# Kernel optimization log

Hardware: AMD Instinct MI355X
Metric: run time of the kernel (lower is better)

## Reference

```python
import jax, jax.numpy as jnp
import numpy as np

B, T, C, H = 4, 2048, 1024, 16
D = C // H  # head dim = 64

def setup_inputs() -> dict:
    key = jax.random.key(0)
    k1, k2, k3 = jax.random.split(key, 3)
    s = 1.0 / np.sqrt(C)
    return {
        "x": jax.random.normal(k1, (B, T, C), dtype=jnp.float32),
        "W_attn": jax.random.normal(k2, (C, 3 * C), dtype=jnp.float32) * s,
        "b_attn": jnp.zeros((3 * C,), dtype=jnp.float32),
        "W_proj": jax.random.normal(k3, (C, C), dtype=jnp.float32) * s,
        "b_proj": jnp.zeros((C,), dtype=jnp.float32),
    }

def reference(x, W_attn, b_attn, W_proj, b_proj):
    qkv = x @ W_attn + b_attn                      # [B,T,3C]
    q, k, v = jnp.split(qkv, 3, axis=-1)
    # [B,T,C] -> [B,H,T,D]
    q = q.reshape(B, T, H, D).transpose(0, 2, 1, 3)
    k = k.reshape(B, T, H, D).transpose(0, 2, 1, 3)
    v = v.reshape(B, T, H, D).transpose(0, 2, 1, 3)
    scale = 1.0 / np.sqrt(D)
    att = jnp.einsum('bhqd,bhkd->bhqk', q, k) * scale   # [B,H,T,T]
    causal = jnp.tril(jnp.ones((T, T), dtype=bool))
    att = jnp.where(causal[None, None], att, jnp.float32(-jnp.inf))
    att = jax.nn.softmax(att, axis=-1)
    y = jnp.einsum('bhqk,bhkd->bhqd', att, v)            # [B,H,T,D]
    y = y.transpose(0, 2, 1, 3).reshape(B, T, C)
    return y @ W_proj + b_proj
```

## Files before the change

kernel.cpp:

```cpp
#include <hip/hip_runtime.h>
#include <cstdint>
#include <cstddef>

typedef __bf16 bf16;
typedef __bf16 bf16x8 __attribute__((ext_vector_type(8)));
typedef __bf16 bf16x4 __attribute__((ext_vector_type(4)));
typedef short  s16x4  __attribute__((ext_vector_type(4)));
typedef float  f32x4  __attribute__((ext_vector_type(4)));

#define MFMA16(a, b, c) __builtin_amdgcn_mfma_f32_16x16x32_bf16((a), (b), (c), 0, 0, 0)

#if __has_builtin(__builtin_amdgcn_mfma_f32_16x16x16bf16_1k)
#define HAVE_K16 1
#else
#define HAVE_K16 0
#endif

#if __has_builtin(__builtin_amdgcn_exp2f)
#define EXP2(x) __builtin_amdgcn_exp2f(x)
#else
#define EXP2(x) exp2f(x)
#endif

constexpr int Bsz = 4;
constexpr int T   = 2048;
constexpr int Cd  = 1024;
constexpr int Hn  = 16;
constexpr int Mrows = Bsz * T;
constexpr int QKV_LD = 3 * Cd;

constexpr float QSCALE = 0.125f * 1.4426950408889634f;

__global__ __launch_bounds__(256) void cvt_f32_bf16(const float* __restrict__ in,
                                                    bf16* __restrict__ out, int n) {
    int i = (blockIdx.x * 256 + threadIdx.x) * 8;
    if (i >= n) return;
    float4 a = *(const float4*)(in + i);
    float4 b = *(const float4*)(in + i + 4);
    bf16x8 o;
    o[0] = (bf16)a.x; o[1] = (bf16)a.y; o[2] = (bf16)a.z; o[3] = (bf16)a.w;
    o[4] = (bf16)b.x; o[5] = (bf16)b.y; o[6] = (bf16)b.z; o[7] = (bf16)b.w;
    *(bf16x8*)(out + i) = o;
}

template <int KDIM, int NDIM>
__global__ __launch_bounds__(256) void transpose_cvt(const float* __restrict__ W,
                                                     bf16* __restrict__ Wt) {
    __shared__ float tile[32][33];
    int k0 = blockIdx.y * 32;
    int n0 = blockIdx.x * 32;
    int tx = threadIdx.x;
    int ty = threadIdx.y;
    #pragma unroll
    for (int r = 0; r < 32; r += 8)
        tile[r + ty][tx] = W[(size_t)(k0 + r + ty) * NDIM + n0 + tx];
    __syncthreads();
    #pragma unroll
    for (int r = 0; r < 32; r += 8)
        Wt[(size_t)(n0 + r + ty) * KDIM + k0 + tx] = (bf16)tile[tx][r + ty];
}

template <int N, bool OUT_BF16>
__global__ __launch_bounds__(256) void gemm_bf16(const bf16* __restrict__ A,
                                                 const bf16* __restrict__ Bt,
                                                 const float* __restrict__ bias,
                                                 void* __restrict__ outp,
                                                 float oscale, int oscale_n) {
    constexpr int K = 1024;
    __shared__ __align__(16) bf16 As[128 * 64];
    __shared__ __align__(16) bf16 Bs[128 * 64];

    const int tid  = threadIdx.x;
    const int w    = tid >> 6;
    const int lane = tid & 63;
    const int wm   = w & 1, wn = w >> 1;
    const int quad = lane >> 4, c16 = lane & 15;

    const int lin = (int)(blockIdx.y * gridDim.x + blockIdx.x);
    const int x8  = lin & 7;
    const int q   = lin >> 3;
    const int m0  = (x8 + 8 * (q & 7)) * 128;
    const int n0  = (q >> 3) * 128;

    const int srow = lane >> 3;
    const int scol = ((lane & 7) ^ srow) * 8;
    const int sw   = c16 & 7;

    f32x4 acc[4][4] = {};

    for (int kt = 0; kt < K / 64; ++kt) {
        const int kk = kt * 64;
        #pragma unroll
        for (int i = 0; i < 4; ++i) {
            const int arow = 32 * w + 8 * i;
            __builtin_amdgcn_global_load_lds(
                (const __attribute__((address_space(1))) void*)(A + (size_t)(m0 + arow + srow) * K + kk + scol),
                (__attribute__((address_space(3))) void*)(&As[arow * 64]),
                16, 0, 0);
            __builtin_amdgcn_global_load_lds(
                (const __attribute__((address_space(1))) void*)(Bt + (size_t)(n0 + arow + srow) * K + kk + scol),
                (__attribute__((address_space(3))) void*)(&Bs[arow * 64]),
                16, 0, 0);
        }
        __syncthreads();

        #pragma unroll
        for (int ks = 0; ks < 2; ++ks) {
            const int go = ((ks * 4 + quad) ^ sw) * 8;
            bf16x8 af[4], bfv[4];
            #pragma unroll
            for (int mb = 0; mb < 4; ++mb)
                af[mb] = *(const bf16x8*)&As[(wm * 64 + mb * 16 + c16) * 64 + go];
            #pragma unroll
            for (int nb = 0; nb < 4; ++nb)
                bfv[nb] = *(const bf16x8*)&Bs[(wn * 64 + nb * 16 + c16) * 64 + go];
            #pragma unroll
            for (int mb = 0; mb < 4; ++mb)
                #pragma unroll
                for (int nb = 0; nb < 4; ++nb)
                    acc[mb][nb] = MFMA16(af[mb], bfv[nb], acc[mb][nb]);
        }
        __syncthreads();
    }

    #pragma unroll
    for (int nb = 0; nb < 4; ++nb) {
        const int n = n0 + wn * 64 + nb * 16 + c16;
        const float bv = bias[n];
        const float sc = (n < oscale_n) ? oscale : 1.0f;
        #pragma unroll
        for (int mb = 0; mb < 4; ++mb) {
            const int mbase = m0 + wm * 64 + mb * 16 + quad * 4;
            #pragma unroll
            for (int r = 0; r < 4; ++r) {
                float v = (acc[mb][nb][r] + bv) * sc;
                if (OUT_BF16)
                    ((bf16*)outp)[(size_t)(mbase + r) * N + n] = (bf16)v;
                else
                    ((float*)outp)[(size_t)(mbase + r) * N + n] = v;
            }
        }
    }
}

__global__ __launch_bounds__(256, 2) void attn_fwd(const bf16* __restrict__ qkv,
                                                   bf16* __restrict__ yp0,
                                                   bf16* __restrict__ yp1,
                                                   float* __restrict__ lp) {
    __shared__ __align__(16) bf16 Ks2[2][4096];
    __shared__ __align__(16) bf16 Vs[2][64 * 64];
#if !HAVE_K16
    __shared__ __align__(16) bf16 Ps[4][32 * 72];
#endif

    const int x    = blockIdx.x;
    const int xq   = x >> 1;
    const int sgl  = x & 1;
    const int h    = blockIdx.y;
    const int bb   = blockIdx.z;
    const int tid  = threadIdx.x;
    const int w    = tid >> 6;
    const int lane = tid & 63;
    const int quad = lane >> 4, c16 = lane & 15;

    const size_t base = (size_t)(bb * T) * QKV_LD;

    const int g = tid >> 5;
    const int p = tid & 31;

    auto vs_store = [&](bf16* vbuf, const bf16x8& va, const bf16x8& vb) {
        #pragma unroll
        for (int j = 0; j < 8; ++j) {
            union { bf16 hh[2]; uint32_t u; } pk;
            pk.hh[0] = va[j]; pk.hh[1] = vb[j];
            const int row = 8 * g + j;
            *(uint32_t*)&vbuf[row * 64 + (((p >> 1) ^ (row & 15)) << 2) + ((p & 1) << 1)] = pk.u;
        }
    };

    bf16* __restrict__ ydst = sgl ? yp1 : yp0;
    float* __restrict__ ldst = lp + (size_t)sgl * Mrows * Hn;

    for (int ph = 0; ph < 2; ++ph) {
        const int qt = ph ? xq : (15 - xq);
        const int q0 = qt * 128;
        const int rowbase = q0 + w * 32;
        const int start = sgl ? (qt + 1) : 0;
        const int nkt = qt + 1;

        __syncthreads();

        {
            const int kb = start * 64;
            #pragma unroll
            for (int ii = 0; ii < 2; ++ii) {
                const int i = 2 * w + ii;
                const bf16* gp = qkv + base + (size_t)(kb + 8 * i + (lane & 7)) * QKV_LD + Cd + h * 64 + (lane >> 3) * 8;
                __builtin_amdgcn_global_load_lds(
                    (const __attribute__((address_space(1))) void*)gp,
                    (__attribute__((address_space(3))) void*)(&Ks2[0][i * 512]), 16, 0, 0);
            }
            const bf16* vp = qkv + base + (size_t)(kb + 2 * p) * QKV_LD + 2 * Cd + h * 64 + g * 8;
            bf16x8 va = *(const bf16x8*)vp;
            bf16x8 vb = *(const bf16x8*)(vp + QKV_LD);
            vs_store(Vs[0], va, vb);
        }

        bf16x8 qf[2][2];
        #pragma unroll
        for (int mb = 0; mb < 2; ++mb) {
            const bf16* qp = qkv + base + (size_t)(rowbase + 16 * mb + c16) * QKV_LD + h * 64 + quad * 8;
            qf[mb][0] = *(const bf16x8*)qp;
            qf[mb][1] = *(const bf16x8*)(qp + 32);
        }

        f32x4 yacc[2][4] = {};
        float lsum[2] = {};

        for (int j = 0; j < nkt; ++j) {
            const int cur = j & 1, nxt = cur ^ 1;
            const int k0 = (start + j) * 64;
            __syncthreads();

            bf16x8 va, vb;
            const bool more = (j + 1 < nkt);
            if (more) {
                const int kn = k0 + 64;
                #pragma unroll
                for (int ii = 0; ii < 2; ++ii) {
                    const int i = 2 * w + ii;
                    const bf16* gp = qkv + base + (size_t)(kn + 8 * i + (lane & 7)) * QKV_LD + Cd + h * 64 + (lane >> 3) * 8;
                    __builtin_amdgcn_global_load_lds(
                        (const __attribute__((address_space(1))) void*)gp,
                        (__attribute__((address_space(3))) void*)(&Ks2[nxt][i * 512]), 16, 0, 0);
                }
                const bf16* vp = qkv + base + (size_t)(kn + 2 * p) * QKV_LD + 2 * Cd + h * 64 + g * 8;
                va = *(const bf16x8*)vp;
                vb = *(const bf16x8*)(vp + QKV_LD);
            }

            if (k0 <= rowbase + 31) {
                f32x4 s[2][4] = {};
                __builtin_amdgcn_s_setprio(1);
                #pragma unroll
                for (int ks = 0; ks < 2; ++ks)
                    #pragma unroll
                    for (int blk = 0; blk < 4; ++blk) {
                        const bf16x8 kf = *(const bf16x8*)
                            &Ks2[cur][(2 * blk + (c16 >> 3)) * 512 + (4 * ks + quad) * 64 + (c16 & 7) * 8];
                        #pragma unroll
                        for (int mb = 0; mb < 2; ++mb)
                            s[mb][blk] = MFMA16(kf, qf[mb][ks], s[mb][blk]);
                    }
                __builtin_amdgcn_s_setprio(0);

#if HAVE_K16
                union B4 { bf16x4 v; s16x4 s; } pb[2][4];
#endif
                #pragma unroll
                for (int mb = 0; mb < 2; ++mb) {
                    const int rb = rowbase + 16 * mb;
                    const int qglob = rb + c16;
                    const bool needMask = (k0 + 63 > rb);
                    #pragma unroll
                    for (int blk = 0; blk < 4; ++blk) {
                        #pragma unroll
                        for (int r = 0; r < 4; ++r) {
                            const int key = k0 + blk * 16 + quad * 4 + r;
                            float e = s[mb][blk][r];
                            if (needMask) e = (key > qglob) ? -INFINITY : e;
                            float pv = EXP2(e);
                            lsum[mb] += pv;
#if HAVE_K16
                            pb[mb][blk].v[r] = (bf16)pv;
#else
                            Ps[w][(mb * 16 + c16) * 72 + blk * 16 + quad * 4 + r] = (bf16)pv;
#endif
                        }
                    }
                }

#if HAVE_K16
                __builtin_amdgcn_s_setprio(1);
                #pragma unroll
                for (int blk = 0; blk < 4; ++blk)
                    #pragma unroll
                    for (int d16 = 0; d16 < 4; ++d16) {
                        union B4u { bf16x4 v; s16x4 s; } vf;
                        vf.v = *(const bf16x4*)
                            &Vs[cur][(d16 * 16 + c16) * 64 + ((((blk << 2) | quad) ^ c16) << 2)];
                        #pragma unroll
                        for (int mb = 0; mb < 2; ++mb)
                            yacc[mb][d16] = __builtin_amdgcn_mfma_f32_16x16x16bf16_1k(
                                vf.s, pb[mb][blk].s, yacc[mb][d16], 0, 0, 0);
                    }
                __builtin_amdgcn_s_setprio(0);
#else
                asm volatile("s_waitcnt lgkmcnt(0)" ::: "memory");
                #pragma unroll
                for (int ks = 0; ks < 2; ++ks) {
                    bf16x8 pf0 = *(const bf16x8*)&Ps[w][(0 * 16 + c16) * 72 + ks * 32 + quad * 8];
                    bf16x8 pf1 = *(const bf16x8*)&Ps[w][(1 * 16 + c16) * 72 + ks * 32 + quad * 8];
                    #pragma unroll
                    for (int d16 = 0; d16 < 4; ++d16) {
                        const int row = d16 * 16 + c16;
                        const int g0 = ks * 8 + quad * 2;
                        bf16x4 lo = *(const bf16x4*)&Vs[cur][row * 64 + ((g0 ^ c16) << 2)];
                        bf16x4 hi = *(const bf16x4*)&Vs[cur][row * 64 + (((g0 + 1) ^ c16) << 2)];
                        bf16x8 vfr;
                        vfr[0] = lo[0]; vfr[1] = lo[1]; vfr[2] = lo[2]; vfr[3] = lo[3];
                        vfr[4] = hi[0]; vfr[5] = hi[1]; vfr[6] = hi[2]; vfr[7] = hi[3];
                        yacc[0][d16] = MFMA16(pf0, vfr, yacc[0][d16]);
                        yacc[1][d16] = MFMA16(pf1, vfr, yacc[1][d16]);
                    }
                }
#endif
            }

            if (more)
                vs_store(Vs[nxt], va, vb);
        }

        #pragma unroll
        for (int mb = 0; mb < 2; ++mb) {
            lsum[mb] += __shfl_xor(lsum[mb], 16);
            lsum[mb] += __shfl_xor(lsum[mb], 32);
        }

#if HAVE_K16
        #pragma unroll
        for (int mb = 0; mb < 2; ++mb) {
            const int row = rowbase + 16 * mb + c16;
            bf16* yw = ydst + (size_t)(bb * T + row) * Cd + h * 64;
            #pragma unroll
            for (int d16 = 0; d16 < 4; ++d16) {
                bf16x4 o;
                #pragma unroll
                for (int r = 0; r < 4; ++r)
                    o[r] = (bf16)(yacc[mb][d16][r]);
                *(bf16x4*)(yw + d16 * 16 + quad * 4) = o;
            }
            if (quad == 0)
                ldst[(size_t)(bb * T + row) * Hn + h] = lsum[mb];
        }
#else
        #pragma unroll
        for (int mb = 0; mb < 2; ++mb)
            #pragma unroll
            for (int r = 0; r < 4; ++r) {
                const float lsv = __shfl(lsum[mb], quad * 4 + r);
                const int row = rowbase + 16 * mb + quad * 4 + r;
                bf16* yw = ydst + (size_t)(bb * T + row) * Cd + h * 64;
                #pragma unroll
                for (int d16 = 0; d16 < 4; ++d16)
                    yw[d16 * 16 + c16] = (bf16)(yacc[mb][d16][r]);
                if (c16 == 0)
                    ldst[(size_t)(bb * T + row) * Hn + h] = lsv;
            }
#endif
    }
}

__global__ __launch_bounds__(256) void attn_combine(const bf16* __restrict__ yp0,
                                                    const bf16* __restrict__ yp1,
                                                    const float* __restrict__ lp,
                                                    bf16* __restrict__ y) {
    int i = (blockIdx.x * 256 + threadIdx.x) * 8;
    int row = i >> 10;
    int hh  = (i & 1023) >> 6;
    float l = lp[(size_t)row * Hn + hh] + lp[(size_t)Mrows * Hn + (size_t)row * Hn + hh];
    float inv = 1.f / l;
    bf16x8 a = *(const bf16x8*)(yp0 + i);
    bf16x8 b = *(const bf16x8*)(yp1 + i);
    bf16x8 o;
    #pragma unroll
    for (int j = 0; j < 8; ++j)
        o[j] = (bf16)(((float)a[j] + (float)b[j]) * inv);
    *(bf16x8*)(y + i) = o;
}

extern "C" void kernel_launch(void* const* d_in, const int* in_sizes, int n_in,
                              void* d_out, int out_size, void* d_ws, size_t ws_size,
                              hipStream_t stream) {
    const float* x      = (const float*)d_in[0];
    const float* W_attn = (const float*)d_in[1];
    const float* b_attn = (const float*)d_in[2];
    const float* W_proj = (const float*)d_in[3];
    const float* b_proj = (const float*)d_in[4];
    float* out = (float*)d_out;

    bf16* xb   = (bf16*)d_ws;
    bf16* Wat  = xb  + (size_t)Mrows * Cd;
    bf16* Wpt  = Wat + (size_t)QKV_LD * Cd;
    bf16* qkv  = Wpt + (size_t)Cd * Cd;
    bf16* yb   = qkv + (size_t)Mrows * QKV_LD;
    bf16* yp1  = yb  + (size_t)Mrows * Cd;
    float* lp  = (float*)(yp1 + (size_t)Mrows * Cd);

    cvt_f32_bf16<<<(Mrows * Cd) / (256 * 8), 256, 0, stream>>>(x, xb, Mrows * Cd);
    transpose_cvt<Cd, QKV_LD><<<dim3(QKV_LD / 32, Cd / 32), dim3(32, 8), 0, stream>>>(W_attn, Wat);
    transpose_cvt<Cd, Cd><<<dim3(Cd / 32, Cd / 32), dim3(32, 8), 0, stream>>>(W_proj, Wpt);

    gemm_bf16<QKV_LD, true><<<dim3(QKV_LD / 128, Mrows / 128), 256, 0, stream>>>(
        xb, Wat, b_attn, qkv, QSCALE, Cd);

    attn_fwd<<<dim3(16, Hn, Bsz), 256, 0, stream>>>(qkv, yb, yp1, lp);
    attn_combine<<<(Mrows * Cd) / (256 * 8), 256, 0, stream>>>(yb, yp1, lp, yb);

    gemm_bf16<Cd, false><<<dim3(Cd / 128, Mrows / 128), 256, 0, stream>>>(
        yb, Wpt, b_proj, out, 1.0f, 0);
}
```

Baseline: 288.4 us.

## Split attention key range three ways per query tile and drop setprio hints

The attention kernel now splits each query tile's causal key range across three blocks instead of two, giving 24 x-blocks per head and batch. Each split writes its own partial output and row sum, and the combine kernel adds all three. The third partial buffer and the row-sum array reuse workspace regions (the bf16 input and the weight-transpose area) that are no longer needed at that point. This is meant to raise block count and balance work across CUs. In exchange it adds combine traffic and extra Q loads per block, and it also removes the s_setprio hints around the MFMA loops.

Measured after the change: 275.6 us. 4.4% less time.

```diff
diff --git a/kernel.cpp b/kernel.cpp
--- a/kernel.cpp
+++ b/kernel.cpp
@@ -146,6 +146,7 @@
 __global__ __launch_bounds__(256, 2) void attn_fwd(const bf16* __restrict__ qkv,
                                                    bf16* __restrict__ yp0,
                                                    bf16* __restrict__ yp1,
+                                                   bf16* __restrict__ yp2,
                                                    float* __restrict__ lp) {
     __shared__ __align__(16) bf16 Ks2[2][4096];
     __shared__ __align__(16) bf16 Vs[2][64 * 64];
@@ -154,8 +155,8 @@
 #endif
 
     const int x    = blockIdx.x;
-    const int xq   = x >> 1;
-    const int sgl  = x & 1;
+    const int xq   = x / 3;
+    const int sgl  = x - 3 * xq;
     const int h    = blockIdx.y;
     const int bb   = blockIdx.z;
     const int tid  = threadIdx.x;
@@ -178,15 +179,20 @@
         }
     };
 
-    bf16* __restrict__ ydst = sgl ? yp1 : yp0;
+    bf16* __restrict__ ydst = (sgl == 0) ? yp0 : ((sgl == 1) ? yp1 : yp2);
     float* __restrict__ ldst = lp + (size_t)sgl * Mrows * Hn;
 
     for (int ph = 0; ph < 2; ++ph) {
         const int qt = ph ? xq : (15 - xq);
         const int q0 = qt * 128;
         const int rowbase = q0 + w * 32;
-        const int start = sgl ? (qt + 1) : 0;
-        const int nkt = qt + 1;
+
+        const int n = 2 * qt + 2;
+        int f0, f1;
+        if (ph == 0) { f0 = (n + 2) / 3; f1 = (n + 1) / 3; }
+        else         { f0 = n / 3;       f1 = (n + 1) / 3; }
+        const int start = (sgl == 0) ? 0 : ((sgl == 1) ? f0 : f0 + f1);
+        const int nkt   = (sgl == 0) ? f0 : ((sgl == 1) ? f1 : n - f0 - f1);
 
         __syncthreads();
 
@@ -241,7 +247,6 @@
 
             if (k0 <= rowbase + 31) {
                 f32x4 s[2][4] = {};
-                __builtin_amdgcn_s_setprio(1);
                 #pragma unroll
                 for (int ks = 0; ks < 2; ++ks)
                     #pragma unroll
@@ -252,7 +257,6 @@
                         for (int mb = 0; mb < 2; ++mb)
                             s[mb][blk] = MFMA16(kf, qf[mb][ks], s[mb][blk]);
                     }
-                __builtin_amdgcn_s_setprio(0);
 
 #if HAVE_K16
                 union B4 { bf16x4 v; s16x4 s; } pb[2][4];
@@ -281,7 +285,6 @@
                 }
 
 #if HAVE_K16
-                __builtin_amdgcn_s_setprio(1);
                 #pragma unroll
                 for (int blk = 0; blk < 4; ++blk)
                     #pragma unroll
@@ -294,7 +297,6 @@
                             yacc[mb][d16] = __builtin_amdgcn_mfma_f32_16x16x16bf16_1k(
                                 vf.s, pb[mb][blk].s, yacc[mb][d16], 0, 0, 0);
                     }
-                __builtin_amdgcn_s_setprio(0);
 #else
                 asm volatile("s_waitcnt lgkmcnt(0)" ::: "memory");
                 #pragma unroll
@@ -363,19 +365,23 @@
 
 __global__ __launch_bounds__(256) void attn_combine(const bf16* __restrict__ yp0,
                                                     const bf16* __restrict__ yp1,
+                                                    const bf16* __restrict__ yp2,
                                                     const float* __restrict__ lp,
                                                     bf16* __restrict__ y) {
     int i = (blockIdx.x * 256 + threadIdx.x) * 8;
     int row = i >> 10;
     int hh  = (i & 1023) >> 6;
-    float l = lp[(size_t)row * Hn + hh] + lp[(size_t)Mrows * Hn + (size_t)row * Hn + hh];
+    const size_t S = (size_t)Mrows * Hn;
+    const size_t li = (size_t)row * Hn + hh;
+    float l = lp[li] + lp[S + li] + lp[2 * S + li];
     float inv = 1.f / l;
     bf16x8 a = *(const bf16x8*)(yp0 + i);
     bf16x8 b = *(const bf16x8*)(yp1 + i);
+    bf16x8 c = *(const bf16x8*)(yp2 + i);
     bf16x8 o;
     #pragma unroll
     for (int j = 0; j < 8; ++j)
-        o[j] = (bf16)(((float)a[j] + (float)b[j]) * inv);
+        o[j] = (bf16)(((float)a[j] + (float)b[j] + (float)c[j]) * inv);
     *(bf16x8*)(y + i) = o;
 }
 
@@ -395,7 +401,8 @@
     bf16* qkv  = Wpt + (size_t)Cd * Cd;
     bf16* yb   = qkv + (size_t)Mrows * QKV_LD;
     bf16* yp1  = yb  + (size_t)Mrows * Cd;
-    float* lp  = (float*)(yp1 + (size_t)Mrows * Cd);
+    bf16*  yp2 = xb;
+    float* lp  = (float*)Wat;
 
     cvt_f32_bf16<<<(Mrows * Cd) / (256 * 8), 256, 0, stream>>>(x, xb, Mrows * Cd);
     transpose_cvt<Cd, QKV_LD><<<dim3(QKV_LD / 32, Cd / 32), dim3(32, 8), 0, stream>>>(W_attn, Wat);
@@ -404,8 +411,8 @@
     gemm_bf16<QKV_LD, true><<<dim3(QKV_LD / 128, Mrows / 128), 256, 0, stream>>>(
         xb, Wat, b_attn, qkv, QSCALE, Cd);
 
-    attn_fwd<<<dim3(16, Hn, Bsz), 256, 0, stream>>>(qkv, yb, yp1, lp);
-    attn_combine<<<(Mrows * Cd) / (256 * 8), 256, 0, stream>>>(yb, yp1, lp, yb);
+    attn_fwd<<<dim3(24, Hn, Bsz), 256, 0, stream>>>(qkv, yb, yp1, yp2, lp);
+    attn_combine<<<(Mrows * Cd) / (256 * 8), 256, 0, stream>>>(yb, yp1, yp2, lp, yb);
 
     gemm_bf16<Cd, false><<<dim3(Cd / 128, Mrows / 128), 256, 0, stream>>>(
         yb, Wpt, b_proj, out, 1.0f, 0);
```
